# Kernel tuning notes

Measured on AMD Instinct MI355X. Metric: run time of the kernel, lower is better.

Reference implementation:

```python
import jax, jax.numpy as jnp
import numpy as np

B, F, S = 64, 1024, 256
H = 1024  # hidden_size == input_size (required by default forward path)


def setup_inputs() -> dict:
    key = jax.random.key(0)
    k1, k2, k3, k4 = jax.random.split(key, 4)
    stdv = 1.0 / (H ** 0.5)
    x = jax.random.normal(k1, (B, F, S), dtype=jnp.float32)
    W = jax.random.uniform(k2, (F, 4 * H), dtype=jnp.float32, minval=-stdv, maxval=stdv)
    U = jax.random.uniform(k3, (H, 4 * H), dtype=jnp.float32, minval=-stdv, maxval=stdv)
    bias = jax.random.uniform(k4, (4 * H,), dtype=jnp.float32, minval=-stdv, maxval=stdv)
    return {"x": x, "W": W, "U": U, "bias": bias}


def reference(x, W, U, bias):
    # x: [B, F, S]. Faithful to MotionLSTM.forward with init_states=None,
    # isSampling=False, output_frame=0:  c_t = f_t * x_t + i_t * g_t.
    batch, _, seq = x.shape
    HS = U.shape[0]
    # Precompute input projection once: [S, B, 4H]
    xW = jnp.einsum('bfs,fg->sbg', x, W)
    x_seq = jnp.transpose(x, (2, 0, 1))  # [S, B, F]
    h0 = jnp.zeros((batch, HS), dtype=x.dtype)
    c0 = jnp.zeros((batch, HS), dtype=x.dtype)

    def step(carry, inputs):
        h, c = carry
        xw_t, x_t = inputs
        gates = xw_t + h @ U + bias  # [B, 4H]
        i_t = jax.nn.sigmoid(gates[:, :HS])
        f_t = jax.nn.sigmoid(gates[:, HS:2 * HS])
        g_t = jnp.tanh(gates[:, 2 * HS:3 * HS])
        o_t = jax.nn.sigmoid(gates[:, 3 * HS:])
        c_new = f_t * x_t + i_t * g_t  # isSampling=False path
        h_new = o_t * jnp.tanh(c_new)
        return (h_new, c_new), h_new

    (h_T, c_T), hs = jax.lax.scan(step, (h0, c0), (xW, x_seq))
    hidden_seq = jnp.transpose(hs, (1, 2, 0))  # [B, H, S]
    return hidden_seq, h_T, c_T
```

## Files before the change

### kernel.cpp

```cpp
#include <hip/hip_runtime.h>
#include <hip/hip_bf16.h>

typedef float f32x4 __attribute__((ext_vector_type(4)));
typedef short short8 __attribute__((ext_vector_type(8)));
typedef __bf16 bf16x8 __attribute__((ext_vector_type(8)));
typedef unsigned int u32x4 __attribute__((ext_vector_type(4)));

#define DI __device__ __forceinline__

constexpr int Bsz = 64;
constexpr int Fd  = 1024;
constexpr int Seq = 256;
constexpr int G4  = 4096;
constexpr int Mrows = Seq * Bsz;

DI float bf2f(unsigned short u) {
  union { unsigned int i; float f; } v; v.i = ((unsigned int)u) << 16; return v.f;
}
DI unsigned short f2bf(float f) {
  union { float ff; unsigned int i; } v; v.ff = f;
  unsigned int x = v.i;
  return (unsigned short)((x + 0x7fffu + ((x >> 16) & 1u)) >> 16);
}
DI float sigm(float x) { return 1.f / (1.f + __expf(-x)); }
DI float tanhfast(float x) {
  float e = __expf(-2.f * fabsf(x));
  float t = (1.f - e) / (1.f + e);
  return x < 0.f ? -t : t;
}
DI f32x4 mfma16(short8 a, short8 b, f32x4 c) {
  return __builtin_amdgcn_mfma_f32_16x16x32_bf16(
      __builtin_bit_cast(bf16x8, a), __builtin_bit_cast(bf16x8, b), c, 0, 0, 0);
}

DI void ld4x4_sys(const unsigned int* p0, const unsigned int* p1,
                  const unsigned int* p2, const unsigned int* p3,
                  u32x4& a, u32x4& b, u32x4& c, u32x4& d) {
  asm volatile(
      "global_load_dwordx4 %0, %4, off sc0 sc1\n\t"
      "global_load_dwordx4 %1, %5, off sc0 sc1\n\t"
      "global_load_dwordx4 %2, %6, off sc0 sc1\n\t"
      "global_load_dwordx4 %3, %7, off sc0 sc1\n\t"
      "s_waitcnt vmcnt(0)"
      : "=&v"(a), "=&v"(b), "=&v"(c), "=&v"(d)
      : "v"(p0), "v"(p1), "v"(p2), "v"(p3)
      : "memory");
}

__global__ void k_tx(const float* __restrict__ x, unsigned short* __restrict__ xs) {
  __shared__ float t[32][33];
  int b = blockIdx.z, f0 = blockIdx.y * 32, s0 = blockIdx.x * 32;
  int tx = threadIdx.x & 31, ty = threadIdx.x >> 5;
  const float* src = x + ((size_t)b * Fd + f0) * Seq + s0;
#pragma unroll
  for (int i = 0; i < 32; i += 8)
    t[ty + i][tx] = src[(size_t)(ty + i) * Seq + tx];
  __syncthreads();
#pragma unroll
  for (int i = 0; i < 32; i += 8) {
    int s = s0 + ty + i, f = f0 + tx;
    xs[((size_t)s * Bsz + b) * Fd + f] = f2bf(t[tx][ty + i]);
  }
}

__global__ void k_tw(const float* __restrict__ in, unsigned short* __restrict__ out) {
  __shared__ float t[32][33];
  int n0 = blockIdx.x * 32, k0 = blockIdx.y * 32;
  int tx = threadIdx.x & 31, ty = threadIdx.x >> 5;
#pragma unroll
  for (int i = 0; i < 32; i += 8)
    t[ty + i][tx] = in[(size_t)(k0 + ty + i) * G4 + n0 + tx];
  __syncthreads();
#pragma unroll
  for (int i = 0; i < 32; i += 8)
    out[(size_t)(n0 + ty + i) * 1024 + k0 + tx] = f2bf(t[tx][ty + i]);
}

__global__ void k_zero(unsigned int* p, int n) {
  int i = blockIdx.x * 256 + threadIdx.x;
  if (i < n) p[i] = 0u;
}

__launch_bounds__(256, 2)
__global__ void k_gemm(const unsigned short* __restrict__ A,
                       const unsigned short* __restrict__ Bt,
                       unsigned short* __restrict__ C) {
  __shared__ unsigned short a_lds[128 * 64];
  __shared__ unsigned short b_lds[128 * 64];
  int bid = blockIdx.x;
  int tm = bid & 127, tn = bid >> 7;
  int tid = threadIdx.x, w = tid >> 6, l = tid & 63;
  int wm = w >> 1, wn = w & 1;
  f32x4 acc[4][4] = {};
  const unsigned short* Ab = A + (size_t)(tm * 128) * 1024;
  const unsigned short* Bb = Bt + (size_t)(tn * 128) * 1024;
  for (int kt = 0; kt < 16; ++kt) {
#pragma unroll
    for (int i = 0; i < 4; ++i) {
      int ci = tid + i * 256;
      int row = ci >> 3;
      int kB = (ci & 7) * 16;
      short8 va = *(const short8*)((const char*)(Ab + (size_t)row * 1024 + kt * 64) + kB);
      short8 vb = *(const short8*)((const char*)(Bb + (size_t)row * 1024 + kt * 64) + kB);
      int dst = row * 128 + (kB ^ ((row & 7) << 4));
      *(short8*)((char*)a_lds + dst) = va;
      *(short8*)((char*)b_lds + dst) = vb;
    }
    __syncthreads();
#pragma unroll
    for (int kb = 0; kb < 2; ++kb) {
      short8 af[4], bfv[4];
      int kByte = (kb * 32 + ((l >> 4) << 3)) * 2;
#pragma unroll
      for (int mi = 0; mi < 4; ++mi) {
        int row = wm * 64 + mi * 16 + (l & 15);
        af[mi] = *(const short8*)((const char*)a_lds + row * 128 + (kByte ^ ((row & 7) << 4)));
      }
#pragma unroll
      for (int ni = 0; ni < 4; ++ni) {
        int row = wn * 64 + ni * 16 + (l & 15);
        bfv[ni] = *(const short8*)((const char*)b_lds + row * 128 + (kByte ^ ((row & 7) << 4)));
      }
#pragma unroll
      for (int mi = 0; mi < 4; ++mi)
#pragma unroll
        for (int ni = 0; ni < 4; ++ni)
          acc[mi][ni] = mfma16(af[mi], bfv[ni], acc[mi][ni]);
    }
    __syncthreads();
  }
#pragma unroll
  for (int mi = 0; mi < 4; ++mi)
#pragma unroll
    for (int ni = 0; ni < 4; ++ni)
#pragma unroll
      for (int r = 0; r < 4; ++r) {
        int m = tm * 128 + wm * 64 + mi * 16 + ((l >> 4) << 2) + r;
        int n = tn * 128 + wn * 64 + ni * 16 + (l & 15);
        C[(size_t)m * G4 + n] = f2bf(acc[mi][ni][r]);
      }
}

__launch_bounds__(512, 2)
__global__ void k_rec(const unsigned short* __restrict__ xs,
                      const unsigned short* __restrict__ xWb,
                      const unsigned short* __restrict__ Ubt,
                      const float* __restrict__ bias,
                      unsigned int* __restrict__ hbuf,
                      unsigned int* __restrict__ tags,
                      float* __restrict__ out) {
  __shared__ unsigned short h_lds[16 * 1024];
  __shared__ float g_lds[16][132];
  __shared__ float obuf[512][9];
  int bid = blockIdx.x;
  int rg = bid & 3, ch = bid >> 2;
  int tid = threadIdx.x, w = tid >> 6, l = tid & 63;
  int g = w >> 1, cs = w & 1;
  int jloc = cs * 16 + (l & 15);
  int ncol = g * 1024 + ch * 32 + jloc;
  int mrow0 = (l >> 4) << 2;

  const unsigned short* Urow = Ubt + (size_t)ncol * 1024;
  short8 ufr[32];
#pragma unroll
  for (int kb = 0; kb < 32; ++kb)
    ufr[kb] = *(const short8*)(Urow + kb * 32 + ((l >> 4) << 3));
  float bias_l = bias[ncol];

  unsigned int* mytags = tags + rg * 32;
  unsigned int* mytag = mytags + ch;

  int prow = tid >> 5, pj = tid & 31;
  int pb = rg * 16 + prow;
  int pjglob = ch * 32 + pj;

  for (int t = 0; t < Seq; ++t) {
    float xw[4];
#pragma unroll
    for (int r = 0; r < 4; ++r)
      xw[r] = bf2f(xWb[((size_t)t * 64 + rg * 16 + mrow0 + r) * G4 + ncol]);
    float xt = bf2f(xs[((size_t)t * 64 + pb) * Fd + pjglob]);

    f32x4 acc0 = {0.f, 0.f, 0.f, 0.f}, acc1 = {0.f, 0.f, 0.f, 0.f};
    if (t > 0) {
      if (tid < 32) {
        while (__hip_atomic_load(&mytags[tid], __ATOMIC_RELAXED,
                                 __HIP_MEMORY_SCOPE_SYSTEM) < (unsigned int)t) {}
      }
      __syncthreads();
      const unsigned int* hp = hbuf + (((t & 1) ^ 1) << 15) + (rg << 13);
      u32x4 h0, h1, h2, h3;
      ld4x4_sys(hp + tid * 4, hp + 2048 + tid * 4, hp + 4096 + tid * 4,
                hp + 6144 + tid * 4, h0, h1, h2, h3);
      __builtin_amdgcn_sched_barrier(0);
      {
        int c0 = tid;        int r0 = c0 >> 7, b0 = (c0 & 127) * 16;
        *(u32x4*)((char*)h_lds + r0 * 2048 + (b0 ^ ((r0 & 7) << 4))) = h0;
        int c1 = tid + 512;  int r1 = c1 >> 7, b1 = (c1 & 127) * 16;
        *(u32x4*)((char*)h_lds + r1 * 2048 + (b1 ^ ((r1 & 7) << 4))) = h1;
        int c2 = tid + 1024; int r2 = c2 >> 7, b2 = (c2 & 127) * 16;
        *(u32x4*)((char*)h_lds + r2 * 2048 + (b2 ^ ((r2 & 7) << 4))) = h2;
        int c3 = tid + 1536; int r3 = c3 >> 7, b3 = (c3 & 127) * 16;
        *(u32x4*)((char*)h_lds + r3 * 2048 + (b3 ^ ((r3 & 7) << 4))) = h3;
      }
      __syncthreads();
      int arow = l & 15;
      const char* abase = (const char*)h_lds + arow * 2048;
      int sw = (arow & 7) << 4;
      int kres = (l >> 4) << 4;
#pragma unroll
      for (int kb = 0; kb < 32; kb += 2) {
        short8 a0 = *(const short8*)(abase + ((kb * 64 + kres) ^ sw));
        acc0 = mfma16(a0, ufr[kb], acc0);
        short8 a1 = *(const short8*)(abase + (((kb + 1) * 64 + kres) ^ sw));
        acc1 = mfma16(a1, ufr[kb + 1], acc1);
      }
    }
#pragma unroll
    for (int r = 0; r < 4; ++r)
      g_lds[mrow0 + r][g * 32 + jloc] = acc0[r] + acc1[r] + xw[r] + bias_l;
    __syncthreads();
    float iv = g_lds[prow][pj];
    float fv = g_lds[prow][32 + pj];
    float gv = g_lds[prow][64 + pj];
    float ov = g_lds[prow][96 + pj];
    float si = sigm(iv), sf = sigm(fv), tg = tanhfast(gv), so = sigm(ov);
    float cval = sf * xt + si * tg;
    float hval = so * tanhfast(cval);
    obuf[tid][t & 7] = hval;
    unsigned int me = f2bf(hval);
    unsigned int ot = (unsigned int)__shfl_xor((int)me, 1) & 0xffffu;
    if ((pj & 1) == 0)
      __hip_atomic_store(hbuf + ((t & 1) << 15) + pb * 512 + (pjglob >> 1),
                         me | (ot << 16), __ATOMIC_RELAXED,
                         __HIP_MEMORY_SCOPE_SYSTEM);
    if (t == Seq - 1) {
      out[(size_t)16777216 + (size_t)pb * 1024 + pjglob] = hval;
      out[(size_t)16777216 + 65536 + (size_t)pb * 1024 + pjglob] = cval;
    }
    asm volatile("s_waitcnt vmcnt(0)" ::: "memory");
    __syncthreads();
    if (tid == 0)
      __hip_atomic_store(mytag, (unsigned int)(t + 1), __ATOMIC_RELAXED,
                         __HIP_MEMORY_SCOPE_SYSTEM);
    if ((t & 7) == 7) {
      float* dst = out + ((size_t)pb * 1024 + pjglob) * Seq + (t - 7);
#pragma unroll
      for (int q = 0; q < 2; ++q) {
        f32x4 v = {obuf[tid][q * 4], obuf[tid][q * 4 + 1],
                   obuf[tid][q * 4 + 2], obuf[tid][q * 4 + 3]};
        *(f32x4*)(dst + q * 4) = v;
      }
    }
  }
}

extern "C" void kernel_launch(void* const* d_in, const int* in_sizes, int n_in,
                              void* d_out, int out_size, void* d_ws, size_t ws_size,
                              hipStream_t stream) {
  const float* x    = (const float*)d_in[0];
  const float* W    = (const float*)d_in[1];
  const float* U    = (const float*)d_in[2];
  const float* bias = (const float*)d_in[3];
  float* out = (float*)d_out;
  char* ws = (char*)d_ws;

  unsigned short* xs  = (unsigned short*)(ws);
  unsigned short* Wbt = (unsigned short*)(ws + (size_t)33554432);
  unsigned short* Ubt = (unsigned short*)(ws + (size_t)41943040);
  unsigned short* xWb = (unsigned short*)(ws + (size_t)50331648);
  unsigned int* hbuf  = (unsigned int*)(ws + (size_t)184549376);
  unsigned int* tags  = (unsigned int*)(ws + (size_t)184811520);

  k_tx<<<dim3(Seq / 32, Fd / 32, Bsz), 256, 0, stream>>>(x, xs);
  k_tw<<<dim3(G4 / 32, 1024 / 32), 256, 0, stream>>>(W, Wbt);
  k_tw<<<dim3(G4 / 32, 1024 / 32), 256, 0, stream>>>(U, Ubt);
  k_zero<<<1, 256, 0, stream>>>(tags, 256);
  k_gemm<<<dim3((Mrows / 128) * (G4 / 128)), 256, 0, stream>>>(xs, Wbt, xWb);
  k_rec<<<dim3(128), 512, 0, stream>>>(xs, xWb, Ubt, bias, hbuf, tags, out);
}
```

Before: 1.026 ms.

## Interleave gate columns so each wave computes full LSTM cells without LDS exchange

Permutes W and U columns so that the four gates of each hidden unit sit side by side. Each MFMA output tile then holds i,f,g,o for one hidden unit, and the cell update can run directly in registers, which drops the g_lds round trip and one block barrier per step. Swaps the MFMA operands so U is the A operand. Switches synchronisation to per-wave tags that readers poll with vector loads and a min-reduction. The cost is eight times more tags to poll and reliance on per-wave stores being visible without a block barrier.

```diff
diff --git a/kernel.cpp b/kernel.cpp
--- a/kernel.cpp
+++ b/kernel.cpp
@@ -5,6 +5,7 @@
 typedef short short8 __attribute__((ext_vector_type(8)));
 typedef __bf16 bf16x8 __attribute__((ext_vector_type(8)));
 typedef unsigned int u32x4 __attribute__((ext_vector_type(4)));
+typedef unsigned int u32x2 __attribute__((ext_vector_type(2)));
 
 #define DI __device__ __forceinline__
 
@@ -32,6 +33,7 @@
   return __builtin_amdgcn_mfma_f32_16x16x32_bf16(
       __builtin_bit_cast(bf16x8, a), __builtin_bit_cast(bf16x8, b), c, 0, 0, 0);
 }
+DI unsigned int umin2(unsigned int a, unsigned int b) { return a < b ? a : b; }
 
 DI void ld4x4_sys(const unsigned int* p0, const unsigned int* p1,
                   const unsigned int* p2, const unsigned int* p3,
@@ -51,10 +53,9 @@
   __shared__ float t[32][33];
   int b = blockIdx.z, f0 = blockIdx.y * 32, s0 = blockIdx.x * 32;
   int tx = threadIdx.x & 31, ty = threadIdx.x >> 5;
-  const float* src = x + ((size_t)b * Fd + f0) * Seq + s0;
 #pragma unroll
   for (int i = 0; i < 32; i += 8)
-    t[ty + i][tx] = src[(size_t)(ty + i) * Seq + tx];
+    t[ty + i][tx] = x[((size_t)b * Fd + f0 + ty + i) * Seq + s0 + tx];
   __syncthreads();
 #pragma unroll
   for (int i = 0; i < 32; i += 8) {
@@ -72,8 +73,11 @@
     t[ty + i][tx] = in[(size_t)(k0 + ty + i) * G4 + n0 + tx];
   __syncthreads();
 #pragma unroll
-  for (int i = 0; i < 32; i += 8)
-    out[(size_t)(n0 + ty + i) * 1024 + k0 + tx] = f2bf(t[tx][ty + i]);
+  for (int i = 0; i < 32; i += 8) {
+    int n = n0 + ty + i;
+    int np = ((n & 1023) << 2) | (n >> 10);
+    out[(size_t)np * 1024 + k0 + tx] = f2bf(t[tx][ty + i]);
+  }
 }
 
 __global__ void k_zero(unsigned int* p, int n) {
@@ -144,55 +148,63 @@
 __launch_bounds__(512, 2)
 __global__ void k_rec(const unsigned short* __restrict__ xs,
                       const unsigned short* __restrict__ xWb,
-                      const unsigned short* __restrict__ Ubt,
+                      const unsigned short* __restrict__ Uperm,
                       const float* __restrict__ bias,
                       unsigned int* __restrict__ hbuf,
                       unsigned int* __restrict__ tags,
                       float* __restrict__ out) {
   __shared__ unsigned short h_lds[16 * 1024];
-  __shared__ float g_lds[16][132];
   __shared__ float obuf[512][9];
   int bid = blockIdx.x;
   int rg = bid & 3, ch = bid >> 2;
   int tid = threadIdx.x, w = tid >> 6, l = tid & 63;
-  int g = w >> 1, cs = w & 1;
-  int jloc = cs * 16 + (l & 15);
-  int ncol = g * 1024 + ch * 32 + jloc;
-  int mrow0 = (l >> 4) << 2;
-
-  const unsigned short* Urow = Ubt + (size_t)ncol * 1024;
+
+  int jglob = ch * 32 + w * 4 + (l >> 4);
+  int b = rg * 16 + (l & 15);
+  int gcbase = ch * 128 + w * 16;
+
+  const unsigned short* up =
+      Uperm + (size_t)(gcbase + (l & 15)) * 1024 + ((l >> 4) << 3);
   short8 ufr[32];
 #pragma unroll
-  for (int kb = 0; kb < 32; ++kb)
-    ufr[kb] = *(const short8*)(Urow + kb * 32 + ((l >> 4) << 3));
-  float bias_l = bias[ncol];
-
-  unsigned int* mytags = tags + rg * 32;
-  unsigned int* mytag = mytags + ch;
-
-  int prow = tid >> 5, pj = tid & 31;
-  int pb = rg * 16 + prow;
-  int pjglob = ch * 32 + pj;
+  for (int kb = 0; kb < 32; ++kb) {
+    asm volatile("global_load_dwordx4 %0, %1, off"
+                 : "=v"(ufr[kb]) : "v"(up + kb * 32));
+  }
+  asm volatile("s_waitcnt vmcnt(0)" ::: "memory");
+
+  float bias_r[4];
+#pragma unroll
+  for (int r = 0; r < 4; ++r) bias_r[r] = bias[r * 1024 + jglob];
+
+  unsigned int* mytags = tags + rg * 256;
+  unsigned int* mytag = mytags + ch * 8 + w;
 
   for (int t = 0; t < Seq; ++t) {
-    float xw[4];
-#pragma unroll
-    for (int r = 0; r < 4; ++r)
-      xw[r] = bf2f(xWb[((size_t)t * 64 + rg * 16 + mrow0 + r) * G4 + ncol]);
-    float xt = bf2f(xs[((size_t)t * 64 + pb) * Fd + pjglob]);
+    u32x2 xwp = *(const u32x2*)(xWb + ((size_t)(t * 64) + b) * G4 + (jglob << 2));
+    float xt = bf2f(xs[((size_t)t * 64 + b) * Fd + jglob]);
 
     f32x4 acc0 = {0.f, 0.f, 0.f, 0.f}, acc1 = {0.f, 0.f, 0.f, 0.f};
     if (t > 0) {
       if (tid < 32) {
-        while (__hip_atomic_load(&mytags[tid], __ATOMIC_RELAXED,
-                                 __HIP_MEMORY_SCOPE_SYSTEM) < (unsigned int)t) {}
+        const unsigned int* tp = mytags + tid * 8;
+        for (;;) {
+          u32x4 ta, tb;
+          asm volatile(
+              "global_load_dwordx4 %0, %2, off sc0 sc1\n\t"
+              "global_load_dwordx4 %1, %2, off offset:16 sc0 sc1\n\t"
+              "s_waitcnt vmcnt(0)"
+              : "=&v"(ta), "=&v"(tb) : "v"(tp) : "memory");
+          unsigned int m = umin2(umin2(umin2(ta[0], ta[1]), umin2(ta[2], ta[3])),
+                                 umin2(umin2(tb[0], tb[1]), umin2(tb[2], tb[3])));
+          if (m >= (unsigned int)t) break;
+        }
       }
       __syncthreads();
       const unsigned int* hp = hbuf + (((t & 1) ^ 1) << 15) + (rg << 13);
       u32x4 h0, h1, h2, h3;
       ld4x4_sys(hp + tid * 4, hp + 2048 + tid * 4, hp + 4096 + tid * 4,
                 hp + 6144 + tid * 4, h0, h1, h2, h3);
-      __builtin_amdgcn_sched_barrier(0);
       {
         int c0 = tid;        int r0 = c0 >> 7, b0 = (c0 & 127) * 16;
         *(u32x4*)((char*)h_lds + r0 * 2048 + (b0 ^ ((r0 & 7) << 4))) = h0;
@@ -204,53 +216,53 @@
         *(u32x4*)((char*)h_lds + r3 * 2048 + (b3 ^ ((r3 & 7) << 4))) = h3;
       }
       __syncthreads();
-      int arow = l & 15;
-      const char* abase = (const char*)h_lds + arow * 2048;
-      int sw = (arow & 7) << 4;
+      int brow = l & 15;
+      const char* bbase = (const char*)h_lds + brow * 2048;
+      int sw = (brow & 7) << 4;
       int kres = (l >> 4) << 4;
 #pragma unroll
       for (int kb = 0; kb < 32; kb += 2) {
-        short8 a0 = *(const short8*)(abase + ((kb * 64 + kres) ^ sw));
-        acc0 = mfma16(a0, ufr[kb], acc0);
-        short8 a1 = *(const short8*)(abase + (((kb + 1) * 64 + kres) ^ sw));
-        acc1 = mfma16(a1, ufr[kb + 1], acc1);
-      }
-    }
-#pragma unroll
-    for (int r = 0; r < 4; ++r)
-      g_lds[mrow0 + r][g * 32 + jloc] = acc0[r] + acc1[r] + xw[r] + bias_l;
-    __syncthreads();
-    float iv = g_lds[prow][pj];
-    float fv = g_lds[prow][32 + pj];
-    float gv = g_lds[prow][64 + pj];
-    float ov = g_lds[prow][96 + pj];
-    float si = sigm(iv), sf = sigm(fv), tg = tanhfast(gv), so = sigm(ov);
+        short8 b0 = *(const short8*)(bbase + ((kb * 64 + kres) ^ sw));
+        acc0 = mfma16(ufr[kb], b0, acc0);
+        short8 b1 = *(const short8*)(bbase + (((kb + 1) * 64 + kres) ^ sw));
+        acc1 = mfma16(ufr[kb + 1], b1, acc1);
+      }
+    }
+    float gi = acc0[0] + acc1[0] + bf2f((unsigned short)(xwp[0] & 0xffffu)) + bias_r[0];
+    float gf = acc0[1] + acc1[1] + bf2f((unsigned short)(xwp[0] >> 16)) + bias_r[1];
+    float gg = acc0[2] + acc1[2] + bf2f((unsigned short)(xwp[1] & 0xffffu)) + bias_r[2];
+    float go = acc0[3] + acc1[3] + bf2f((unsigned short)(xwp[1] >> 16)) + bias_r[3];
+    float si = sigm(gi), sf = sigm(gf), tg = tanhfast(gg), so = sigm(go);
     float cval = sf * xt + si * tg;
     float hval = so * tanhfast(cval);
+    unsigned int hb = f2bf(hval);
+    unsigned int p1 = (unsigned int)__shfl((int)hb, (l & 15) + 16);
+    unsigned int p2 = (unsigned int)__shfl((int)hb, (l & 15) + 32);
+    unsigned int p3 = (unsigned int)__shfl((int)hb, (l & 15) + 48);
+    if (l < 16) {
+      u32x2 d; d[0] = hb | (p1 << 16); d[1] = p2 | (p3 << 16);
+      unsigned int* hp2 = hbuf + ((t & 1) << 15) +
+                          (unsigned)(rg * 16 + l) * 512 + (ch * 16 + w * 2);
+      asm volatile("global_store_dwordx2 %0, %1, off sc0 sc1"
+                   :: "v"(hp2), "v"(d) : "memory");
+    }
+    asm volatile("s_waitcnt vmcnt(0)" ::: "memory");
+    if (l == 0)
+      asm volatile("global_store_dword %0, %1, off sc0 sc1"
+                   :: "v"(mytag), "v"((unsigned int)(t + 1)) : "memory");
     obuf[tid][t & 7] = hval;
-    unsigned int me = f2bf(hval);
-    unsigned int ot = (unsigned int)__shfl_xor((int)me, 1) & 0xffffu;
-    if ((pj & 1) == 0)
-      __hip_atomic_store(hbuf + ((t & 1) << 15) + pb * 512 + (pjglob >> 1),
-                         me | (ot << 16), __ATOMIC_RELAXED,
-                         __HIP_MEMORY_SCOPE_SYSTEM);
-    if (t == Seq - 1) {
-      out[(size_t)16777216 + (size_t)pb * 1024 + pjglob] = hval;
-      out[(size_t)16777216 + 65536 + (size_t)pb * 1024 + pjglob] = cval;
-    }
-    asm volatile("s_waitcnt vmcnt(0)" ::: "memory");
-    __syncthreads();
-    if (tid == 0)
-      __hip_atomic_store(mytag, (unsigned int)(t + 1), __ATOMIC_RELAXED,
-                         __HIP_MEMORY_SCOPE_SYSTEM);
     if ((t & 7) == 7) {
-      float* dst = out + ((size_t)pb * 1024 + pjglob) * Seq + (t - 7);
+      float* dst = out + ((size_t)b * 1024 + jglob) * Seq + (t - 7);
 #pragma unroll
       for (int q = 0; q < 2; ++q) {
         f32x4 v = {obuf[tid][q * 4], obuf[tid][q * 4 + 1],
                    obuf[tid][q * 4 + 2], obuf[tid][q * 4 + 3]};
         *(f32x4*)(dst + q * 4) = v;
       }
+    }
+    if (t == Seq - 1) {
+      out[(size_t)16777216 + (size_t)b * 1024 + jglob] = hval;
+      out[(size_t)16777216 + 65536 + (size_t)b * 1024 + jglob] = cval;
     }
   }
 }
@@ -265,17 +277,17 @@
   float* out = (float*)d_out;
   char* ws = (char*)d_ws;
 
-  unsigned short* xs  = (unsigned short*)(ws);
-  unsigned short* Wbt = (unsigned short*)(ws + (size_t)33554432);
-  unsigned short* Ubt = (unsigned short*)(ws + (size_t)41943040);
-  unsigned short* xWb = (unsigned short*)(ws + (size_t)50331648);
-  unsigned int* hbuf  = (unsigned int*)(ws + (size_t)184549376);
-  unsigned int* tags  = (unsigned int*)(ws + (size_t)184811520);
+  unsigned short* xs    = (unsigned short*)(ws);
+  unsigned short* Wperm = (unsigned short*)(ws + (size_t)33554432);
+  unsigned short* Uperm = (unsigned short*)(ws + (size_t)41943040);
+  unsigned short* xWb   = (unsigned short*)(ws + (size_t)50331648);
+  unsigned int* hbuf    = (unsigned int*)(ws + (size_t)184549376);
+  unsigned int* tags    = (unsigned int*)(ws + (size_t)184811520);
 
   k_tx<<<dim3(Seq / 32, Fd / 32, Bsz), 256, 0, stream>>>(x, xs);
-  k_tw<<<dim3(G4 / 32, 1024 / 32), 256, 0, stream>>>(W, Wbt);
-  k_tw<<<dim3(G4 / 32, 1024 / 32), 256, 0, stream>>>(U, Ubt);
-  k_zero<<<1, 256, 0, stream>>>(tags, 256);
-  k_gemm<<<dim3((Mrows / 128) * (G4 / 128)), 256, 0, stream>>>(xs, Wbt, xWb);
-  k_rec<<<dim3(128), 512, 0, stream>>>(xs, xWb, Ubt, bias, hbuf, tags, out);
-}
+  k_tw<<<dim3(G4 / 32, 1024 / 32), 256, 0, stream>>>(W, Wperm);
+  k_tw<<<dim3(G4 / 32, 1024 / 32), 256, 0, stream>>>(U, Uperm);
+  k_zero<<<4, 256, 0, stream>>>(tags, 1024);
+  k_gemm<<<dim3((Mrows / 128) * (G4 / 128)), 256, 0, stream>>>(xs, Wperm, xWb);
+  k_rec<<<dim3(128), 512, 0, stream>>>(xs, xWb, Uperm, bias, hbuf, tags, out);
+}
```

After: 1.620 ms. 1.58x slower.
